# Optimization experiments

Measured on AMD Instinct MI355X. Metric: run time of the kernel, lower is better.

## Reference

```python
import jax, jax.numpy as jnp
import numpy as np

# ---- hash-grid constants (from tcnn Encoding config in __init__) ----
N_LEVELS = 16
F = 2                      # n_features_per_level
LOG2_T = 19
T = 1 << LOG2_T            # hashmap entries per level
BASE_RES = 16
PER_LEVEL_SCALE = 1.447269237440378
PRIMES = np.array([1, 2654435761, 805459861], dtype=np.uint32)
# corner offsets of the unit cube, shape [8, 3]
OFFS = np.stack(np.meshgrid([0, 1], [0, 1], [0, 1], indexing='ij'), -1).reshape(8, 3)


def hash_grid_encode(x01, table):
    """x01: [N,3] in [0,1]; table: [L, T, F]. Returns [N, L*F]."""
    offs = jnp.asarray(OFFS, dtype=jnp.int32)          # [8,3]
    primes = jnp.asarray(PRIMES)                       # [3] uint32
    feats = []
    for l in range(N_LEVELS):
        scale = BASE_RES * (PER_LEVEL_SCALE ** l) - 1.0   # tcnn grid scale
        res = int(np.ceil(scale)) + 1                      # grid resolution
        pos = x01 * scale + 0.5                            # [N,3]
        pos0 = jnp.floor(pos)
        w = pos - pos0                                     # trilinear fracs [N,3]
        pos0 = pos0.astype(jnp.int32)
        corners = jnp.clip(pos0[:, None, :] + offs[None], 0, res - 1)  # [N,8,3]
        if res ** 3 <= T:
            # dense (stride) indexing fits in the table
            idx = (corners[..., 0]
                   + res * corners[..., 1]
                   + res * res * corners[..., 2]).astype(jnp.int32)    # [N,8]
        else:
            # spatial hash with uint32 wraparound multiply + xor
            cu = corners.astype(jnp.uint32)
            idx = ((cu[..., 0] * primes[0])
                   ^ (cu[..., 1] * primes[1])
                   ^ (cu[..., 2] * primes[2])) & jnp.uint32(T - 1)
            idx = idx.astype(jnp.int32)
        # trilinear weights: prod over dims of (w if offset==1 else 1-w)
        wc = jnp.where(offs[None].astype(bool), w[:, None, :], 1.0 - w[:, None, :])
        wc = wc.prod(-1)                                   # [N,8]
        g = table[l][idx]                                  # gather -> [N,8,F]
        feats.append(jnp.einsum('nc,ncf->nf', wc, g))      # [N,F]
    return jnp.concatenate(feats, -1)                      # [N, L*F]


def mlp2(x, w1, w2):
    # 2-layer bias-free MLP with ReLU, matching MLP(num_layers=2, bias=False)
    return jnp.maximum(x @ w1, 0.0) @ w2


def setup_inputs() -> dict:
    key = jax.random.key(0)
    ks = jax.random.split(key, 6)
    N = 1048576
    points = jax.random.uniform(ks[0], (N, 3), jnp.float32, -1.0, 1.0)  # in bbox [-1,1]^3
    # tcnn hash-grid init: uniform(-1e-4, 1e-4)
    hash_table = jax.random.uniform(ks[1], (N_LEVELS, T, F), jnp.float32, -1e-4, 1e-4)
    enc_dim = N_LEVELS * F  # 32
    dw1 = jax.random.normal(ks[2], (enc_dim, 64), jnp.float32) * (1.0 / np.sqrt(enc_dim))
    dw2 = jax.random.normal(ks[3], (64, 1), jnp.float32) * (1.0 / 8.0)
    fw1 = jax.random.normal(ks[4], (enc_dim, 64), jnp.float32) * (1.0 / np.sqrt(enc_dim))
    fw2 = jax.random.normal(ks[5], (64, 3), jnp.float32) * (1.0 / 8.0)
    return {"points": points, "hash_table": hash_table,
            "dw1": dw1, "dw2": dw2, "fw1": fw1, "fw2": fw2}


def reference(points, hash_table, dw1, dw2, fw1, fw2):
    # contract_to_unisphere with bbox [[-1,-1,-1],[1,1,1]] -> [0,1]^3, clamped
    x01 = jnp.clip((points + 1.0) * 0.5, 0.0, 1.0)
    enc = hash_grid_encode(x01, hash_table)               # [N, 32]
    density = jax.nn.softplus(mlp2(enc, dw1, dw2))        # [N, 1]
    color = jax.nn.sigmoid(mlp2(enc, fw1, fw2))           # [N, 3]
    return color, density
```

## Files before the change

kernel.cpp:

```cpp
#include <hip/hip_runtime.h>
#include <hip/hip_bf16.h>
#include <cmath>

#define NLV 16
#define TBL_SIZE (1u << 19)
#define NB (1 << 18)

struct LevelConsts {
    float scale[NLV];
    int   res[NLV];
    int   dense[NLV];
};

__device__ __forceinline__ unsigned int f32_to_bf16_rne(float f) {
    unsigned int u = __float_as_uint(f);
    return (u + 0x7FFFu + ((u >> 16) & 1u)) >> 16;
}
__device__ __forceinline__ unsigned int pack_bf16(float a, float b) {
    return f32_to_bf16_rne(a) | (f32_to_bf16_rne(b) << 16);
}
__device__ __forceinline__ short f32_to_bf16_s(float f) {
    return (short)f32_to_bf16_rne(f);
}
__device__ __forceinline__ float bf16lo_to_f32(unsigned int g) {
    return __uint_as_float(g << 16);
}
__device__ __forceinline__ float bf16hi_to_f32(unsigned int g) {
    return __uint_as_float(g & 0xFFFF0000u);
}

typedef __attribute__((ext_vector_type(8))) short bf16x8;
typedef __attribute__((ext_vector_type(4))) float f32x4;
typedef __attribute__((ext_vector_type(2))) unsigned int u32x2;
typedef __attribute__((ext_vector_type(4))) unsigned int u32x4;

__global__ __launch_bounds__(256) void cvt_table(const float* __restrict__ in,
                                                 unsigned int* __restrict__ out, int npairs) {
    int n2 = npairs >> 1;
    int i = blockIdx.x * 256 + threadIdx.x;
    int stride = gridDim.x * 256;
    const f32x4* in4 = (const f32x4*)in;
    u32x2* out2 = (u32x2*)out;
    for (; i < n2; i += stride) {
        f32x4 v = __builtin_nontemporal_load(&in4[i]);
        u32x2 o;
        o.x = pack_bf16(v.x, v.y);
        o.y = pack_bf16(v.z, v.w);
        __builtin_nontemporal_store(o, &out2[i]);
    }
}

__device__ __forceinline__ unsigned spread3(unsigned x) {
    x &= 0x3FFu;
    x = (x | (x << 16)) & 0x030000FFu;
    x = (x | (x << 8))  & 0x0300F00Fu;
    x = (x | (x << 4))  & 0x030C30C3u;
    x = (x | (x << 2))  & 0x09249249u;
    return x;
}
__device__ __forceinline__ unsigned bucket_key(float px, float py, float pz) {
    float x = fminf(fmaxf((px + 1.0f) * 0.5f, 0.0f), 1.0f);
    float y = fminf(fmaxf((py + 1.0f) * 0.5f, 0.0f), 1.0f);
    float z = fminf(fmaxf((pz + 1.0f) * 0.5f, 0.0f), 1.0f);
    int ix = min((int)(x * 64.0f), 63);
    int iy = min((int)(y * 64.0f), 63);
    int iz = min((int)(z * 64.0f), 63);
    return spread3((unsigned)ix) | (spread3((unsigned)iy) << 1) | (spread3((unsigned)iz) << 2);
}

__global__ __launch_bounds__(256) void zero_u32(unsigned* __restrict__ p, int n) {
    int i = blockIdx.x * 256 + threadIdx.x;
    if (i < n) p[i] = 0u;
}

__global__ __launch_bounds__(256) void bucket_hist(const float* __restrict__ pts,
                                                   unsigned* __restrict__ hist, int N) {
    int i = blockIdx.x * 256 + threadIdx.x;
    int stride = gridDim.x * 256;
    for (; i < N; i += stride) {
        float px = pts[3 * i + 0];
        float py = pts[3 * i + 1];
        float pz = pts[3 * i + 2];
        atomicAdd(&hist[bucket_key(px, py, pz)], 1u);
    }
}

__device__ __forceinline__ unsigned block_excl_scan_256(unsigned v, unsigned* wtot) {
    int t = threadIdx.x;
    int lane = t & 63, wid = t >> 6;
    unsigned x = v;
#pragma unroll
    for (int d = 1; d < 64; d <<= 1) {
        unsigned y = __shfl_up(x, d, 64);
        if (lane >= d) x += y;
    }
    unsigned wex = x - v;
    if (lane == 63) wtot[wid] = x;
    __syncthreads();
    if (t == 0) {
        unsigned r = 0;
        for (int i = 0; i < 4; i++) { unsigned tt = wtot[i]; wtot[i] = r; r += tt; }
    }
    __syncthreads();
    return wex + wtot[wid];
}

__global__ __launch_bounds__(256) void scan1(const unsigned* __restrict__ hist,
                                             unsigned* __restrict__ base,
                                             unsigned* __restrict__ bsum) {
    __shared__ unsigned wtot[4];
    int t = threadIdx.x, b = blockIdx.x;
    unsigned v = hist[b * 256 + t];
    unsigned ex = block_excl_scan_256(v, wtot);
    base[b * 256 + t] = ex;
    if (t == 255) bsum[b] = ex + v;
}

__global__ __launch_bounds__(256) void scan2(unsigned* __restrict__ bsum) {
    __shared__ unsigned wtot[4];
    int t = threadIdx.x;
    unsigned s[4];
    unsigned tot = 0;
#pragma unroll
    for (int j = 0; j < 4; j++) { s[j] = bsum[4 * t + j]; tot += s[j]; }
    unsigned ex = block_excl_scan_256(tot, wtot);
    unsigned run = ex;
#pragma unroll
    for (int j = 0; j < 4; j++) { unsigned sv = s[j]; bsum[4 * t + j] = run; run += sv; }
}

__global__ __launch_bounds__(256) void scan3(unsigned* __restrict__ base,
                                             const unsigned* __restrict__ bsum) {
    base[blockIdx.x * 256 + threadIdx.x] += bsum[blockIdx.x];
}

__global__ __launch_bounds__(256) void bucket_scatter(const float* __restrict__ pts,
                                                      unsigned* __restrict__ base,
                                                      float* __restrict__ spts,
                                                      unsigned* __restrict__ perm, int N) {
    int i = blockIdx.x * 256 + threadIdx.x;
    int stride = gridDim.x * 256;
    for (; i < N; i += stride) {
        float px = pts[3 * i + 0];
        float py = pts[3 * i + 1];
        float pz = pts[3 * i + 2];
        unsigned k = bucket_key(px, py, pz);
        unsigned pos = atomicAdd(&base[k], 1u);
        spts[3 * pos + 0] = px;
        spts[3 * pos + 1] = py;
        spts[3 * pos + 2] = pz;
        perm[pos] = (unsigned)i;
    }
}

#define ENC_P 4
__global__ __launch_bounds__(256) void encode_lvl(
    const float* __restrict__ points,
    const unsigned int* __restrict__ tbl,
    unsigned int* __restrict__ enc,
    int N, LevelConsts C)
{
    const int level = blockIdx.y;
    const float sc    = C.scale[level];
    const int   res   = C.res[level];
    const int   dense = C.dense[level];
    const unsigned int* __restrict__ t = tbl + (size_t)level * TBL_SIZE;
    unsigned int* __restrict__ eo = enc + (size_t)level * N;

    const int base = blockIdx.x * (256 * ENC_P) + threadIdx.x;

    int   pt[ENC_P];
    int   valid[ENC_P];
    float wx[ENC_P], wy[ENC_P], wz[ENC_P];
    unsigned int i0a[ENC_P][4], i1a[ENC_P][4];

#pragma unroll
    for (int q = 0; q < ENC_P; q++) {
        pt[q] = base + q * 256;
        valid[q] = pt[q] < N;
        int p = valid[q] ? pt[q] : 0;
        float px = __builtin_nontemporal_load(&points[p * 3 + 0]);
        float py = __builtin_nontemporal_load(&points[p * 3 + 1]);
        float pz = __builtin_nontemporal_load(&points[p * 3 + 2]);
        float x = fminf(fmaxf((px + 1.0f) * 0.5f, 0.0f), 1.0f);
        float y = fminf(fmaxf((py + 1.0f) * 0.5f, 0.0f), 1.0f);
        float z = fminf(fmaxf((pz + 1.0f) * 0.5f, 0.0f), 1.0f);

        float fx = x * sc + 0.5f;
        float fy = y * sc + 0.5f;
        float fz = z * sc + 0.5f;
        float f0x = floorf(fx), f0y = floorf(fy), f0z = floorf(fz);
        wx[q] = fx - f0x; wy[q] = fy - f0y; wz[q] = fz - f0z;
        int ix0 = min(max((int)f0x, 0), res - 1);
        int iy0 = min(max((int)f0y, 0), res - 1);
        int iz0 = min(max((int)f0z, 0), res - 1);
        int ix1 = min(ix0 + 1, res - 1);
        int iy1 = min(iy0 + 1, res - 1);
        int iz1 = min(iz0 + 1, res - 1);

#pragma unroll
        for (int m = 0; m < 4; m++) {
            unsigned int uy = (unsigned int)((m & 1) ? iy1 : iy0);
            unsigned int uz = (unsigned int)((m & 2) ? iz1 : iz0);
            unsigned int i0, i1;
            if (dense) {
                unsigned int b = (unsigned int)res * uy + (unsigned int)(res * res) * uz;
                i0 = (unsigned int)ix0 + b;
                i1 = (unsigned int)ix1 + b;
            } else {
                unsigned int H = uy * 2654435761u ^ uz * 805459861u;
                i0 = ((unsigned int)ix0 ^ H) & (TBL_SIZE - 1u);
                i1 = ((unsigned int)ix1 ^ H) & (TBL_SIZE - 1u);
            }
            i0a[q][m] = i0;
            i1a[q][m] = i1;
        }
    }

    u32x2       pr[ENC_P][4];
    unsigned int ex[ENC_P][4];
#pragma unroll
    for (int q = 0; q < ENC_P; q++) {
#pragma unroll
        for (int m = 0; m < 4; m++) {
            unsigned int i0 = i0a[q][m], i1 = i1a[q][m];
            pr[q][m] = *(const u32x2*)(t + (i0 & ~1u));
            unsigned int eidx = (i1 == (i0 ^ 1u)) ? i0 : i1;
            ex[q][m] = t[eidx];
        }
    }

#pragma unroll
    for (int q = 0; q < ENC_P; q++) {
        float e0 = 0.0f, e1 = 0.0f;
        float wxq = wx[q];
#pragma unroll
        for (int m = 0; m < 4; m++) {
            unsigned int i0 = i0a[q][m], i1 = i1a[q][m];
            u32x2 P = pr[q][m];
            unsigned int v0   = (i0 & 1u) ? P.y : P.x;
            unsigned int vpar = (i0 & 1u) ? P.x : P.y;
            unsigned int v1   = (i1 == (i0 ^ 1u)) ? vpar : ex[q][m];
            float wyz = (((m & 1) ? wy[q] : 1.0f - wy[q])) *
                        (((m & 2) ? wz[q] : 1.0f - wz[q]));
            float w0 = wyz * (1.0f - wxq);
            float w1 = wyz * wxq;
            e0 = fmaf(w0, bf16lo_to_f32(v0), e0);
            e0 = fmaf(w1, bf16lo_to_f32(v1), e0);
            e1 = fmaf(w0, bf16hi_to_f32(v0), e1);
            e1 = fmaf(w1, bf16hi_to_f32(v1), e1);
        }
        if (valid[q]) __builtin_nontemporal_store(pack_bf16(e0, e1), &eo[pt[q]]);
    }
}

__global__ __launch_bounds__(256, 4) void mlp_kernel(
    const unsigned int* __restrict__ enc,
    const float* __restrict__ dw1, const float* __restrict__ dw2,
    const float* __restrict__ fw1, const float* __restrict__ fw2,
    const unsigned int* __restrict__ perm,
    float* __restrict__ out, int N, int ntiles)
{
    __shared__ unsigned int hsh[4][16][68];
    __shared__ float sOut[4][256];

    const int tid  = threadIdx.x;
    const int wave = tid >> 6;
    const int lane = tid & 63;
    const int l15 = lane & 15;
    const int quad = lane >> 4;

    bf16x8 B1[8];
#pragma unroll
    for (int nt = 0; nt < 8; nt++) {
        int col = nt * 16 + l15;
        const float* w = (col < 64) ? (dw1 + col) : (fw1 + (col - 64));
#pragma unroll
        for (int j = 0; j < 8; j++) {
            int k = quad * 8 + j;
            B1[nt][j] = f32_to_bf16_s(w[k * 64]);
        }
    }

    bf16x8 B2[4];
#pragma unroll
    for (int s = 0; s < 4; s++) {
#pragma unroll
        for (int j = 0; j < 8; j++) {
            int k_lds = s * 32 + quad * 8 + j;
            int hu = ((k_lds & 7) << 4) | (k_lds >> 3);
            float v = 0.0f;
            if (l15 == 0)      v = (hu < 64)  ? dw2[hu] : 0.0f;
            else if (l15 < 4)  v = (hu >= 64) ? fw2[(hu - 64) * 3 + (l15 - 1)] : 0.0f;
            B2[s][j] = f32_to_bf16_s(v);
        }
    }

    for (int tile = blockIdx.x; tile < ntiles; tile += gridDim.x) {
        const int wbase = tile * 256 + wave * 64;

        unsigned int au[4][4];
#pragma unroll
        for (int sub = 0; sub < 4; sub++) {
            int ptc = min(wbase + sub * 16 + l15, N - 1);
#pragma unroll
            for (int j = 0; j < 4; j++)
                au[sub][j] = enc[(size_t)(quad * 4 + j) * N + ptc];
        }

#pragma unroll
        for (int sub = 0; sub < 4; sub++) {
            union { unsigned int u[4]; bf16x8 v; } acvt;
#pragma unroll
            for (int j = 0; j < 4; j++) acvt.u[j] = au[sub][j];

            f32x4 acc1[8];
#pragma unroll
            for (int nt = 0; nt < 8; nt++) {
                acc1[nt] = (f32x4){0.0f, 0.0f, 0.0f, 0.0f};
                acc1[nt] = __builtin_amdgcn_mfma_f32_16x16x32_bf16(acvt.v, B1[nt], acc1[nt], 0, 0, 0);
            }

#pragma unroll
            for (int r = 0; r < 4; r++) {
                u32x4 pk;
#pragma unroll
                for (int d = 0; d < 4; d++) {
                    float h0 = fmaxf(acc1[2 * d + 0][r], 0.0f);
                    float h1 = fmaxf(acc1[2 * d + 1][r], 0.0f);
                    pk[d] = pack_bf16(h0, h1);
                }
                *(u32x4*)&hsh[wave][quad * 4 + r][l15 * 4] = pk;
            }

            f32x4 p0 = (f32x4){0,0,0,0}, p1 = (f32x4){0,0,0,0};
            f32x4 p2 = (f32x4){0,0,0,0}, p3 = (f32x4){0,0,0,0};
            {
                bf16x8 a0 = *(const bf16x8*)&hsh[wave][l15][0 * 16 + quad * 4];
                bf16x8 a1 = *(const bf16x8*)&hsh[wave][l15][1 * 16 + quad * 4];
                bf16x8 a2 = *(const bf16x8*)&hsh[wave][l15][2 * 16 + quad * 4];
                bf16x8 a3 = *(const bf16x8*)&hsh[wave][l15][3 * 16 + quad * 4];
                p0 = __builtin_amdgcn_mfma_f32_16x16x32_bf16(a0, B2[0], p0, 0, 0, 0);
                p1 = __builtin_amdgcn_mfma_f32_16x16x32_bf16(a1, B2[1], p1, 0, 0, 0);
                p2 = __builtin_amdgcn_mfma_f32_16x16x32_bf16(a2, B2[2], p2, 0, 0, 0);
                p3 = __builtin_amdgcn_mfma_f32_16x16x32_bf16(a3, B2[3], p3, 0, 0, 0);
            }
            f32x4 acc2;
#pragma unroll
            for (int r = 0; r < 4; r++) acc2[r] = (p0[r] + p1[r]) + (p2[r] + p3[r]);

            if (l15 < 4) {
#pragma unroll
                for (int r = 0; r < 4; r++)
                    sOut[wave][(sub * 16 + quad * 4 + r) * 4 + l15] = acc2[r];
            }
        }

        if (perm) {
            int p = wbase + lane;
            if (p < N) {
                unsigned int o = perm[p];
                f32x4 v = *(const f32x4*)&sOut[wave][lane * 4];
                float d = v[0];
                d = (d > 20.0f) ? d : log1pf(expf(d));
                out[(size_t)3 * N + o] = d;
                float r0 = 1.0f / (1.0f + expf(-v[1]));
                float g0 = 1.0f / (1.0f + expf(-v[2]));
                float b0 = 1.0f / (1.0f + expf(-v[3]));
                out[(size_t)o * 3 + 0] = r0;
                out[(size_t)o * 3 + 1] = g0;
                out[(size_t)o * 3 + 2] = b0;
            }
        } else {
            long long cmax = ((long long)N - wbase) * 3;
#pragma unroll
            for (int round = 0; round < 3; round++) {
                int f = round * 64 + lane;
                int lp = f / 3, c = f - lp * 3;
                float v = sOut[wave][lp * 4 + 1 + c];
                v = 1.0f / (1.0f + expf(-v));
                if (f < cmax) out[(size_t)wbase * 3 + f] = v;
            }
            {
                int p = wbase + lane;
                float v = sOut[wave][lane * 4];
                v = (v > 20.0f) ? v : log1pf(expf(v));
                if (p < N) out[(size_t)3 * N + p] = v;
            }
        }
    }
}

__global__ __launch_bounds__(256) void nerf_fused(
    const float* __restrict__ points,
    const float* __restrict__ table,
    const float* __restrict__ dw1, const float* __restrict__ dw2,
    const float* __restrict__ fw1, const float* __restrict__ fw2,
    float* __restrict__ out, int N, LevelConsts C)
{
    __shared__ float sD[64 * 32];
    __shared__ float sF[64 * 32];
    __shared__ float sDw2[64];
    __shared__ float sFw2[64 * 3];

    for (int idx = threadIdx.x; idx < 2048; idx += 256) {
        int i = idx >> 6;
        int j = idx & 63;
        sD[j * 32 + i] = dw1[idx];
        sF[j * 32 + i] = fw1[idx];
    }
    if (threadIdx.x < 64)  sDw2[threadIdx.x] = dw2[threadIdx.x];
    if (threadIdx.x < 192) sFw2[threadIdx.x] = fw2[threadIdx.x];
    __syncthreads();

    int gid = blockIdx.x * 256 + threadIdx.x;
    if (gid >= N) return;

    float px = points[gid * 3 + 0];
    float py = points[gid * 3 + 1];
    float pz = points[gid * 3 + 2];
    float x = fminf(fmaxf((px + 1.0f) * 0.5f, 0.0f), 1.0f);
    float y = fminf(fmaxf((py + 1.0f) * 0.5f, 0.0f), 1.0f);
    float z = fminf(fmaxf((pz + 1.0f) * 0.5f, 0.0f), 1.0f);

    float enc[32];

#pragma unroll
    for (int l = 0; l < NLV; l++) {
        const float sc = C.scale[l];
        const int   res = C.res[l];
        const int   dense = C.dense[l];
        const float* __restrict__ tbl = table + (size_t)l * TBL_SIZE * 2;

        float fx = x * sc + 0.5f;
        float fy = y * sc + 0.5f;
        float fz = z * sc + 0.5f;
        float f0x = floorf(fx), f0y = floorf(fy), f0z = floorf(fz);
        float wx = fx - f0x, wy = fy - f0y, wz = fz - f0z;
        int ix0 = min(max((int)f0x, 0), res - 1);
        int iy0 = min(max((int)f0y, 0), res - 1);
        int iz0 = min(max((int)f0z, 0), res - 1);
        int ix1 = min(ix0 + 1, res - 1);
        int iy1 = min(iy0 + 1, res - 1);
        int iz1 = min(iz0 + 1, res - 1);

        float e0 = 0.0f, e1 = 0.0f;
#pragma unroll
        for (int c = 0; c < 8; c++) {
            int cx = (c & 4) ? ix1 : ix0;
            int cy = (c & 2) ? iy1 : iy0;
            int cz = (c & 1) ? iz1 : iz0;
            float wgt = (((c & 4) ? wx : 1.0f - wx) *
                         ((c & 2) ? wy : 1.0f - wy)) *
                         ((c & 1) ? wz : 1.0f - wz);
            unsigned int idx;
            if (dense) {
                idx = (unsigned int)(cx + res * cy + res * res * cz);
            } else {
                idx = ((unsigned int)cx * 1u
                     ^ (unsigned int)cy * 2654435761u
                     ^ (unsigned int)cz * 805459861u) & (TBL_SIZE - 1u);
            }
            const float2 g = *(const float2*)(tbl + (size_t)idx * 2);
            e0 = fmaf(wgt, g.x, e0);
            e1 = fmaf(wgt, g.y, e1);
        }
        enc[2 * l + 0] = e0;
        enc[2 * l + 1] = e1;
    }

    float dacc = 0.0f, c0 = 0.0f, c1 = 0.0f, c2 = 0.0f;
    for (int j = 0; j < 64; j++) {
        float hd = 0.0f, hf = 0.0f;
        const float* __restrict__ colD = &sD[j * 32];
        const float* __restrict__ colF = &sF[j * 32];
#pragma unroll
        for (int i = 0; i < 32; i++) {
            hd = fmaf(enc[i], colD[i], hd);
            hf = fmaf(enc[i], colF[i], hf);
        }
        hd = fmaxf(hd, 0.0f);
        hf = fmaxf(hf, 0.0f);
        dacc = fmaf(hd, sDw2[j], dacc);
        c0 = fmaf(hf, sFw2[j * 3 + 0], c0);
        c1 = fmaf(hf, sFw2[j * 3 + 1], c1);
        c2 = fmaf(hf, sFw2[j * 3 + 2], c2);
    }

    float density = (dacc > 20.0f) ? dacc : log1pf(expf(dacc));
    out[gid * 3 + 0] = 1.0f / (1.0f + expf(-c0));
    out[gid * 3 + 1] = 1.0f / (1.0f + expf(-c1));
    out[gid * 3 + 2] = 1.0f / (1.0f + expf(-c2));
    out[(size_t)3 * N + gid] = density;
}

extern "C" void kernel_launch(void* const* d_in, const int* in_sizes, int n_in,
                              void* d_out, int out_size, void* d_ws, size_t ws_size,
                              hipStream_t stream) {
    const float* points = (const float*)d_in[0];
    const float* table  = (const float*)d_in[1];
    const float* dw1    = (const float*)d_in[2];
    const float* dw2    = (const float*)d_in[3];
    const float* fw1    = (const float*)d_in[4];
    const float* fw2    = (const float*)d_in[5];
    int N = in_sizes[0] / 3;

    LevelConsts C;
    for (int l = 0; l < NLV; l++) {
        double s = 16.0 * pow(1.447269237440378, (double)l) - 1.0;
        C.scale[l] = (float)s;
        int res = (int)ceil(s) + 1;
        C.res[l] = res;
        C.dense[l] = ((long long)res * res * res <= (long long)TBL_SIZE) ? 1 : 0;
    }

    auto align256 = [](size_t x) { return (x + 255) & ~(size_t)255; };
    const size_t tbl_bytes  = align256((size_t)NLV * TBL_SIZE * 4);
    const size_t enc_bytes  = align256((size_t)N * NLV * 4);
    const size_t spts_bytes = align256((size_t)N * 3 * 4);
    const size_t perm_bytes = align256((size_t)N * 4);
    const size_t hist_bytes = align256((size_t)NB * 4);
    const size_t base_bytes = align256((size_t)NB * 4);
    const size_t bsum_bytes = align256((size_t)(NB / 256) * 4);
    const size_t sort_total = tbl_bytes + enc_bytes + spts_bytes + perm_bytes
                            + hist_bytes + base_bytes + bsum_bytes;

    if (ws_size >= sort_total) {
        char* wp = (char*)d_ws;
        unsigned int* tbl_bf16 = (unsigned int*)wp;            wp += tbl_bytes;
        unsigned int* enc_ws   = (unsigned int*)wp;            wp += enc_bytes;
        float*        spts     = (float*)wp;                   wp += spts_bytes;
        unsigned int* perm     = (unsigned int*)wp;            wp += perm_bytes;
        unsigned int* hist     = (unsigned int*)wp;            wp += hist_bytes;
        unsigned int* base     = (unsigned int*)wp;            wp += base_bytes;
        unsigned int* bsum     = (unsigned int*)wp;            wp += bsum_bytes;

        int npairs = NLV * TBL_SIZE;
        cvt_table<<<1024, 256, 0, stream>>>(table, tbl_bf16, npairs);

        int pblocks = min((N + 255) / 256, 2048);
        zero_u32<<<NB / 256, 256, 0, stream>>>(hist, NB);
        bucket_hist<<<pblocks, 256, 0, stream>>>(points, hist, N);
        scan1<<<NB / 256, 256, 0, stream>>>(hist, base, bsum);
        scan2<<<1, 256, 0, stream>>>(bsum);
        scan3<<<NB / 256, 256, 0, stream>>>(base, bsum);
        bucket_scatter<<<pblocks, 256, 0, stream>>>(points, base, spts, perm, N);

        int chunks = (N + 256 * ENC_P - 1) / (256 * ENC_P);
        encode_lvl<<<dim3(chunks, NLV), 256, 0, stream>>>(spts, tbl_bf16, enc_ws, N, C);

        int ntiles = (N + 255) / 256;
        mlp_kernel<<<1792, 256, 0, stream>>>(enc_ws, dw1, dw2, fw1, fw2, perm,
                                             (float*)d_out, N, ntiles);
    } else if (ws_size >= tbl_bytes + enc_bytes) {
        unsigned int* tbl_bf16 = (unsigned int*)d_ws;
        unsigned int* enc_ws   = (unsigned int*)((char*)d_ws + tbl_bytes);

        int npairs = NLV * TBL_SIZE;
        cvt_table<<<1024, 256, 0, stream>>>(table, tbl_bf16, npairs);

        int chunks = (N + 256 * ENC_P - 1) / (256 * ENC_P);
        encode_lvl<<<dim3(chunks, NLV), 256, 0, stream>>>(points, tbl_bf16, enc_ws, N, C);

        int ntiles = (N + 255) / 256;
        mlp_kernel<<<1792, 256, 0, stream>>>(enc_ws, dw1, dw2, fw1, fw2, nullptr,
                                             (float*)d_out, N, ntiles);
    } else {
        int blocks = (N + 255) / 256;
        nerf_fused<<<blocks, 256, 0, stream>>>(points, table, dw1, dw2, fw1, fw2,
                                               (float*)d_out, N, C);
    }
}
```

Measured before the change: 563.7 us.

## Pack sorted points with permutation index, fold hist zeroing, split gather loads

Bucket scatter now writes each sorted point as one 16-byte record (xyz plus original index) instead of separate xyz and perm arrays. The encode kernel reads it with a single vector load, and the MLP kernel reads the permutation from the fourth lane. The histogram zeroing is folded into the table-conversion kernel, which removes one launch. The gather loop is split so all pair loads are issued before the extra-corner loads, and the extra load is skipped when both corners share a pair. The nontemporal hint on point loads is dropped, and the record layout adds a fourth word per point.

```diff
diff --git a/kernel.cpp b/kernel.cpp
--- a/kernel.cpp
+++ b/kernel.cpp
@@ -35,7 +35,12 @@
 typedef __attribute__((ext_vector_type(4))) unsigned int u32x4;
 
 __global__ __launch_bounds__(256) void cvt_table(const float* __restrict__ in,
-                                                 unsigned int* __restrict__ out, int npairs) {
+                                                 unsigned int* __restrict__ out, int npairs,
+                                                 unsigned int* __restrict__ hist) {
+    if (hist) {
+        int h = blockIdx.x * 256 + threadIdx.x;
+        if (h < NB) hist[h] = 0u;
+    }
     int n2 = npairs >> 1;
     int i = blockIdx.x * 256 + threadIdx.x;
     int stride = gridDim.x * 256;
@@ -68,11 +73,6 @@
     return spread3((unsigned)ix) | (spread3((unsigned)iy) << 1) | (spread3((unsigned)iz) << 2);
 }
 
-__global__ __launch_bounds__(256) void zero_u32(unsigned* __restrict__ p, int n) {
-    int i = blockIdx.x * 256 + threadIdx.x;
-    if (i < n) p[i] = 0u;
-}
-
 __global__ __launch_bounds__(256) void bucket_hist(const float* __restrict__ pts,
                                                    unsigned* __restrict__ hist, int N) {
     int i = blockIdx.x * 256 + threadIdx.x;
@@ -136,8 +136,7 @@
 
 __global__ __launch_bounds__(256) void bucket_scatter(const float* __restrict__ pts,
                                                       unsigned* __restrict__ base,
-                                                      float* __restrict__ spts,
-                                                      unsigned* __restrict__ perm, int N) {
+                                                      f32x4* __restrict__ spts4, int N) {
     int i = blockIdx.x * 256 + threadIdx.x;
     int stride = gridDim.x * 256;
     for (; i < N; i += stride) {
@@ -146,14 +145,14 @@
         float pz = pts[3 * i + 2];
         unsigned k = bucket_key(px, py, pz);
         unsigned pos = atomicAdd(&base[k], 1u);
-        spts[3 * pos + 0] = px;
-        spts[3 * pos + 1] = py;
-        spts[3 * pos + 2] = pz;
-        perm[pos] = (unsigned)i;
+        f32x4 o;
+        o.x = px; o.y = py; o.z = pz; o.w = __uint_as_float((unsigned)i);
+        spts4[pos] = o;
     }
 }
 
 #define ENC_P 4
+template<int PSTRIDE>
 __global__ __launch_bounds__(256) void encode_lvl(
     const float* __restrict__ points,
     const unsigned int* __restrict__ tbl,
@@ -179,9 +178,15 @@
         pt[q] = base + q * 256;
         valid[q] = pt[q] < N;
         int p = valid[q] ? pt[q] : 0;
-        float px = __builtin_nontemporal_load(&points[p * 3 + 0]);
-        float py = __builtin_nontemporal_load(&points[p * 3 + 1]);
-        float pz = __builtin_nontemporal_load(&points[p * 3 + 2]);
+        float px, py, pz;
+        if (PSTRIDE == 4) {
+            f32x4 v = *(const f32x4*)&points[(size_t)p * 4];
+            px = v.x; py = v.y; pz = v.z;
+        } else {
+            px = points[p * 3 + 0];
+            py = points[p * 3 + 1];
+            pz = points[p * 3 + 2];
+        }
         float x = fminf(fmaxf((px + 1.0f) * 0.5f, 0.0f), 1.0f);
         float y = fminf(fmaxf((py + 1.0f) * 0.5f, 0.0f), 1.0f);
         float z = fminf(fmaxf((pz + 1.0f) * 0.5f, 0.0f), 1.0f);
@@ -217,18 +222,23 @@
         }
     }
 
-    u32x2       pr[ENC_P][4];
+    u32x2 pr[ENC_P][4];
+#pragma unroll
+    for (int q = 0; q < ENC_P; q++)
+#pragma unroll
+        for (int m = 0; m < 4; m++)
+            pr[q][m] = *(const u32x2*)(t + (i0a[q][m] & ~1u));
+
     unsigned int ex[ENC_P][4];
 #pragma unroll
-    for (int q = 0; q < ENC_P; q++) {
+    for (int q = 0; q < ENC_P; q++)
 #pragma unroll
         for (int m = 0; m < 4; m++) {
             unsigned int i0 = i0a[q][m], i1 = i1a[q][m];
-            pr[q][m] = *(const u32x2*)(t + (i0 & ~1u));
-            unsigned int eidx = (i1 == (i0 ^ 1u)) ? i0 : i1;
-            ex[q][m] = t[eidx];
-        }
-    }
+            unsigned int e = 0u;
+            if (i1 != (i0 ^ 1u)) e = t[i1];
+            ex[q][m] = e;
+        }
 
 #pragma unroll
     for (int q = 0; q < ENC_P; q++) {
@@ -359,7 +369,7 @@
         if (perm) {
             int p = wbase + lane;
             if (p < N) {
-                unsigned int o = perm[p];
+                unsigned int o = perm[(size_t)p * 4 + 3];
                 f32x4 v = *(const f32x4*)&sOut[wave][lane * 4];
                 float d = v[0];
                 d = (d > 20.0f) ? d : log1pf(expf(d));
@@ -517,50 +527,49 @@
     auto align256 = [](size_t x) { return (x + 255) & ~(size_t)255; };
     const size_t tbl_bytes  = align256((size_t)NLV * TBL_SIZE * 4);
     const size_t enc_bytes  = align256((size_t)N * NLV * 4);
-    const size_t spts_bytes = align256((size_t)N * 3 * 4);
-    const size_t perm_bytes = align256((size_t)N * 4);
+    const size_t spts_bytes = align256((size_t)N * 4 * 4);
     const size_t hist_bytes = align256((size_t)NB * 4);
     const size_t base_bytes = align256((size_t)NB * 4);
     const size_t bsum_bytes = align256((size_t)(NB / 256) * 4);
-    const size_t sort_total = tbl_bytes + enc_bytes + spts_bytes + perm_bytes
+    const size_t sort_total = tbl_bytes + enc_bytes + spts_bytes
                             + hist_bytes + base_bytes + bsum_bytes;
 
     if (ws_size >= sort_total) {
         char* wp = (char*)d_ws;
         unsigned int* tbl_bf16 = (unsigned int*)wp;            wp += tbl_bytes;
         unsigned int* enc_ws   = (unsigned int*)wp;            wp += enc_bytes;
-        float*        spts     = (float*)wp;                   wp += spts_bytes;
-        unsigned int* perm     = (unsigned int*)wp;            wp += perm_bytes;
+        f32x4*        spts4    = (f32x4*)wp;                   wp += spts_bytes;
         unsigned int* hist     = (unsigned int*)wp;            wp += hist_bytes;
         unsigned int* base     = (unsigned int*)wp;            wp += base_bytes;
         unsigned int* bsum     = (unsigned int*)wp;            wp += bsum_bytes;
 
         int npairs = NLV * TBL_SIZE;
-        cvt_table<<<1024, 256, 0, stream>>>(table, tbl_bf16, npairs);
+        cvt_table<<<1024, 256, 0, stream>>>(table, tbl_bf16, npairs, hist);
 
         int pblocks = min((N + 255) / 256, 2048);
-        zero_u32<<<NB / 256, 256, 0, stream>>>(hist, NB);
         bucket_hist<<<pblocks, 256, 0, stream>>>(points, hist, N);
         scan1<<<NB / 256, 256, 0, stream>>>(hist, base, bsum);
         scan2<<<1, 256, 0, stream>>>(bsum);
         scan3<<<NB / 256, 256, 0, stream>>>(base, bsum);
-        bucket_scatter<<<pblocks, 256, 0, stream>>>(points, base, spts, perm, N);
+        bucket_scatter<<<pblocks, 256, 0, stream>>>(points, base, spts4, N);
 
         int chunks = (N + 256 * ENC_P - 1) / (256 * ENC_P);
-        encode_lvl<<<dim3(chunks, NLV), 256, 0, stream>>>(spts, tbl_bf16, enc_ws, N, C);
+        encode_lvl<4><<<dim3(chunks, NLV), 256, 0, stream>>>((const float*)spts4,
+                                                             tbl_bf16, enc_ws, N, C);
 
         int ntiles = (N + 255) / 256;
-        mlp_kernel<<<1792, 256, 0, stream>>>(enc_ws, dw1, dw2, fw1, fw2, perm,
+        mlp_kernel<<<1792, 256, 0, stream>>>(enc_ws, dw1, dw2, fw1, fw2,
+                                             (const unsigned int*)spts4,
                                              (float*)d_out, N, ntiles);
     } else if (ws_size >= tbl_bytes + enc_bytes) {
         unsigned int* tbl_bf16 = (unsigned int*)d_ws;
         unsigned int* enc_ws   = (unsigned int*)((char*)d_ws + tbl_bytes);
 
         int npairs = NLV * TBL_SIZE;
-        cvt_table<<<1024, 256, 0, stream>>>(table, tbl_bf16, npairs);
+        cvt_table<<<1024, 256, 0, stream>>>(table, tbl_bf16, npairs, nullptr);
 
         int chunks = (N + 256 * ENC_P - 1) / (256 * ENC_P);
-        encode_lvl<<<dim3(chunks, NLV), 256, 0, stream>>>(points, tbl_bf16, enc_ws, N, C);
+        encode_lvl<3><<<dim3(chunks, NLV), 256, 0, stream>>>(points, tbl_bf16, enc_ws, N, C);
 
         int ntiles = (N + 255) / 256;
         mlp_kernel<<<1792, 256, 0, stream>>>(enc_ws, dw1, dw2, fw1, fw2, nullptr,
```

After: 567.7 us. Within noise of the previous version (+0.7%).
